# Kernel tuning notes

Measured on AMD Instinct MI355X. Metric: run time of the kernel, lower is better.

## Reference

```python
import jax, jax.numpy as jnp
import numpy as np

N_NODES = 50000


def gcn_conv(x, src, dst, norm, W, b, n_nodes):
    """One GCNConv layer: out = scatter_add(norm * (x @ W)[src] -> dst) + b.
    src/dst already include self loops; norm is the symmetric D^-1/2 A_hat D^-1/2 edge weight."""
    h = x @ W  # [N, C_out]
    msg = h[src] * norm[:, None]  # [E+N, C_out]
    out = jax.ops.segment_sum(msg, dst, num_segments=n_nodes)
    return out + b


def build_norm(edge_index, n_nodes):
    """Add self loops and compute symmetric GCN normalization (PyG GCNConv default)."""
    loop = jnp.arange(n_nodes, dtype=edge_index.dtype)
    src = jnp.concatenate([edge_index[0], loop])
    dst = jnp.concatenate([edge_index[1], loop])
    deg = jax.ops.segment_sum(jnp.ones_like(dst, dtype=jnp.float32), dst, num_segments=n_nodes)
    dinv = jnp.where(deg > 0, jax.lax.rsqrt(jnp.maximum(deg, 1.0)), 0.0)
    norm = dinv[src] * dinv[dst]
    return src, dst, norm


def setup_inputs() -> dict:
    key = jax.random.key(0)
    ks = jax.random.split(key, 8)
    in_c, h1, h2, out_c = 768, 256, 128, 2
    x = jax.random.normal(ks[0], (N_NODES, in_c), dtype=jnp.float32)
    edge_index = jax.random.randint(ks[1], (2, 800000), 0, N_NODES, dtype=jnp.int32)
    W1 = jax.random.normal(ks[2], (in_c, h1), dtype=jnp.float32) * 0.02
    b1 = jnp.zeros((h1,), dtype=jnp.float32)
    W2 = jax.random.normal(ks[3], (h1, h2), dtype=jnp.float32) * 0.02
    b2 = jnp.zeros((h2,), dtype=jnp.float32)
    W3 = jax.random.normal(ks[4], (h2, out_c), dtype=jnp.float32) * 0.02
    b3 = jnp.zeros((out_c,), dtype=jnp.float32)
    return {"x": x, "edge_index": edge_index, "W1": W1, "b1": b1,
            "W2": W2, "b2": b2, "W3": W3, "b3": b3}


def reference(x, edge_index, W1, b1, W2, b2, W3, b3):
    n = x.shape[0]
    src, dst, norm = build_norm(edge_index, n)
    # Dropout is identity in eval mode (training=False), so it is omitted.
    h = jax.nn.relu(gcn_conv(x, src, dst, norm, W1, b1, n))
    h = jax.nn.relu(gcn_conv(h, src, dst, norm, W2, b2, n))
    h = gcn_conv(h, src, dst, norm, W3, b3, n)
    return jax.nn.sigmoid(h)
```

## Files before the change

### kernel.cpp

```cpp
#include <hip/hip_runtime.h>
#include <math.h>

typedef short s16x8 __attribute__((ext_vector_type(8)));
typedef __bf16 b16x8 __attribute__((ext_vector_type(8)));
typedef float f32x4 __attribute__((ext_vector_type(4)));
typedef float f32x2 __attribute__((ext_vector_type(2)));
typedef unsigned int u32x4 __attribute__((ext_vector_type(4)));

__device__ inline short f2bf(float f) {
    unsigned u = __float_as_uint(f);
    unsigned r = u + 0x7FFFu + ((u >> 16) & 1u);
    return (short)(r >> 16);
}
__device__ inline float bf2f(unsigned short u) {
    return __uint_as_float(((unsigned)u) << 16);
}


__device__ inline void make_wt_elem(const float* __restrict__ W, short* __restrict__ Wt,
                                    int K, int N, int idx) {
    int NB = N >> 7;
    int j = idx & 7;
    int l = (idx >> 3) & 63;
    int nt = (idx >> 9) & 7;
    int rest = idx >> 12;
    int b = rest % NB;
    int c = rest / NB;
    int k = c * 32 + (l >> 4) * 8 + j;
    int n = b * 128 + nt * 16 + (l & 15);
    Wt[idx] = f2bf(W[(size_t)k * N + n]);
}

__global__ void prep_kernel(const int* __restrict__ dst, int* __restrict__ cnt, int E,
                            const float* __restrict__ W1, short* __restrict__ Wt1,
                            const float* __restrict__ W2, short* __restrict__ Wt2,
                            int cb, int w1b) {
    int b = blockIdx.x;
    int tid = threadIdx.x;
    if (b < cb) {
        int e = b * 256 + tid;
        if (e < E) atomicAdd(&cnt[dst[e]], 1);
    } else if (b < cb + w1b) {
        int idx = (b - cb) * 256 + tid;
        make_wt_elem(W1, Wt1, 768, 256, idx);
    } else {
        int idx = (b - cb - w1b) * 256 + tid;
        make_wt_elem(W2, Wt2, 256, 128, idx);
    }
}


__global__ __launch_bounds__(1024) void blockscan_kernel(const int* __restrict__ cnt,
                                                         int* __restrict__ rp,
                                                         int* __restrict__ bsum, int n) {
    __shared__ int sdata[1024];
    int tid = threadIdx.x;
    int i = blockIdx.x * 1024 + tid;
    int v = (i < n) ? cnt[i] : 0;
    sdata[tid] = v;
    __syncthreads();
    for (int off = 1; off < 1024; off <<= 1) {
        int t = 0;
        if (tid >= off) t = sdata[tid - off];
        __syncthreads();
        sdata[tid] += t;
        __syncthreads();
    }
    if (i < n) rp[i] = sdata[tid] - v;
    if (tid == 1023) bsum[blockIdx.x] = sdata[1023];
}

__global__ void topscan_kernel(int* bsum, int nb) {
    int lane = threadIdx.x;
    int carry = 0;
    for (int base = 0; base < nb; base += 64) {
        int idx = base + lane;
        int orig = (idx < nb) ? bsum[idx] : 0;
        int v = orig;
        for (int off = 1; off < 64; off <<= 1) {
            int t = __shfl_up(v, off, 64);
            if (lane >= off) v += t;
        }
        if (idx < nb) bsum[idx] = carry + v - orig;
        carry += __shfl(v, 63, 64);
    }
}

__global__ __launch_bounds__(1024) void fixup_kernel(int* __restrict__ rp,
                                                     const int* __restrict__ bsum,
                                                     const int* __restrict__ cnt,
                                                     int* __restrict__ cursor,
                                                     float* __restrict__ dinv,
                                                     int n, int E) {
    int i = blockIdx.x * 1024 + threadIdx.x;
    if (i < n) {
        int r = rp[i] + bsum[blockIdx.x];
        rp[i] = r;
        cursor[i] = r;
        dinv[i] = rsqrtf((float)cnt[i] + 1.0f);
    }
    if (i == 0) rp[n] = E;
}

__global__ void fill_kernel(const int* __restrict__ src, const int* __restrict__ dst,
                            int* __restrict__ cursor, const float* __restrict__ dinv,
                            int* __restrict__ csrc, float* __restrict__ cw, int E) {
    int e = blockIdx.x * blockDim.x + threadIdx.x;
    if (e >= E) return;
    int d = dst[e];
    int s = src[e];
    int p = atomicAdd(&cursor[d], 1);
    csrc[p] = s;
    cw[p] = dinv[s] * dinv[d];
}


__global__ __launch_bounds__(256, 3) void gemm1_kernel(const float* __restrict__ x,
                                                       const short* __restrict__ Wt,
                                                       unsigned char* __restrict__ h8,
                                                       int M) {
    constexpr int KC = 24;
    constexpr int RT = 2;
    constexpr int O = KC * 4;
    constexpr int F = KC * RT * 64 / 256;

    __shared__ s16x8 As[KC * RT * 64];

    const int tid = threadIdx.x;
    const int m0 = blockIdx.x * (RT * 16);

    s16x8 v[F];
#pragma unroll
    for (int i = 0; i < F; ++i) {
        int idx = i * 256 + tid;
        int r = idx / O;
        int o = idx - r * O;
        int row = m0 + r;
        if (row >= M) row = M - 1;
        const float4* fp = (const float4*)(x + (size_t)row * 768 + o * 8);
        float4 f0 = fp[0];
        float4 f1 = fp[1];
        u32x4 pk;
        pk.x = (__float_as_uint(f0.x) >> 16) | (__float_as_uint(f0.y) & 0xFFFF0000u);
        pk.y = (__float_as_uint(f0.z) >> 16) | (__float_as_uint(f0.w) & 0xFFFF0000u);
        pk.z = (__float_as_uint(f1.x) >> 16) | (__float_as_uint(f1.y) & 0xFFFF0000u);
        pk.w = (__float_as_uint(f1.z) >> 16) | (__float_as_uint(f1.w) & 0xFFFF0000u);
        v[i] = __builtin_bit_cast(s16x8, pk);
    }
#pragma unroll
    for (int i = 0; i < F; ++i) {
        int idx = i * 256 + tid;
        int r = idx / O;
        int o = idx - r * O;
        int c = o >> 2, q = o & 3;
        int slot = q * 16 + (((r & 15) + q + ((c & 3) << 2)) & 15);
        As[(c * RT + (r >> 4)) * 64 + slot] = v[i];
    }
    __syncthreads();

    const int lane = tid & 63;
    const int wave = tid >> 6;
    const int b128 = wave >> 1;
    const int nt0 = (wave & 1) * 4;
    const int q = lane >> 4;
    const int rl = lane & 15;
    const s16x8* wt = (const s16x8*)Wt;

    f32x4 acc[RT][4];
#pragma unroll
    for (int i = 0; i < RT; ++i)
#pragma unroll
        for (int j = 0; j < 4; ++j)
            acc[i][j] = (f32x4){0.f, 0.f, 0.f, 0.f};

#pragma unroll 4
    for (int c = 0; c < KC; ++c) {
        int slot = q * 16 + ((rl + q + ((c & 3) << 2)) & 15);
        b16x8 areg[RT], breg[4];
#pragma unroll
        for (int i = 0; i < RT; ++i)
            areg[i] = __builtin_bit_cast(b16x8, As[(c * RT + i) * 64 + slot]);
        size_t bb = (size_t)(c * 2 + b128) * 512 + nt0 * 64 + lane;
#pragma unroll
        for (int j = 0; j < 4; ++j)
            breg[j] = __builtin_bit_cast(b16x8, wt[bb + j * 64]);
#pragma unroll
        for (int i = 0; i < RT; ++i)
#pragma unroll
            for (int j = 0; j < 4; ++j)
                acc[i][j] = __builtin_amdgcn_mfma_f32_16x16x32_bf16(areg[i], breg[j], acc[i][j], 0, 0, 0);
    }

    const int quad = lane >> 4;
    const int nl = lane & 15;
#pragma unroll
    for (int i = 0; i < RT; ++i) {
        int rbase = m0 + i * 16 + quad * 4;
#pragma unroll
        for (int j = 0; j < 4; ++j) {
            int col = wave * 64 + j * 16 + nl;
#pragma unroll
            for (int r = 0; r < 4; ++r) {
                int row = rbase + r;
                if (row < M) {
                    unsigned u = __builtin_amdgcn_cvt_pk_fp8_f32(acc[i][j][r], acc[i][j][r], 0, false);
                    h8[(size_t)row * 256 + col] = (unsigned char)(u & 0xFF);
                }
            }
        }
    }
}


template<typename AT, int KC, int RT, int CW, int MINW>
__global__ __launch_bounds__(256, MINW) void gemm_panel_kernel(
        const AT* __restrict__ A, const short* __restrict__ Wt,
        unsigned short* __restrict__ Cb, int M) {
    constexpr int K = KC * 32;
    constexpr int O = KC * 4;
    constexpr int F = KC * RT / 4;
    constexpr int NCOLS = CW * 64;
    constexpr int NB = NCOLS >> 7;
    constexpr int MT = RT * CW / 4;

    __shared__ s16x8 As[KC * RT * 64];

    const int tid = threadIdx.x;
    const int m0 = blockIdx.x * (RT * 16);

    s16x8 v[F];
#pragma unroll
    for (int i = 0; i < F; ++i) {
        int idx = i * 256 + tid;
        int r = idx / O;
        int o = idx - r * O;
        int row = m0 + r;
        if (row >= M) row = M - 1;
        v[i] = *(const s16x8*)((const unsigned short*)A + (size_t)row * K + o * 8);
    }
#pragma unroll
    for (int i = 0; i < F; ++i) {
        int idx = i * 256 + tid;
        int r = idx / O;
        int o = idx - r * O;
        int c = o >> 2, q = o & 3;
        int slot = q * 16 + (((r & 15) + q + ((c & 3) << 2)) & 15);
        As[(c * RT + (r >> 4)) * 64 + slot] = v[i];
    }
    __syncthreads();

    const int lane = tid & 63;
    const int wave = tid >> 6;
    const int cw_i = wave % CW;
    const int rg = wave / CW;
    const int mtb = rg * MT;
    const int b128 = (cw_i * 64) >> 7;
    const int nt0 = (cw_i * 4) & 7;
    const int q = lane >> 4;
    const int rl = lane & 15;
    const s16x8* wt = (const s16x8*)Wt;

    f32x4 acc[MT][4];
#pragma unroll
    for (int i = 0; i < MT; ++i)
#pragma unroll
        for (int j = 0; j < 4; ++j)
            acc[i][j] = (f32x4){0.f, 0.f, 0.f, 0.f};

#pragma unroll 4
    for (int c = 0; c < KC; ++c) {
        int slot = q * 16 + ((rl + q + ((c & 3) << 2)) & 15);
        b16x8 areg[MT], breg[4];
#pragma unroll
        for (int i = 0; i < MT; ++i)
            areg[i] = __builtin_bit_cast(b16x8, As[(c * RT + mtb + i) * 64 + slot]);
        size_t bb = (size_t)(c * NB + b128) * 512 + nt0 * 64 + lane;
#pragma unroll
        for (int j = 0; j < 4; ++j)
            breg[j] = __builtin_bit_cast(b16x8, wt[bb + j * 64]);
#pragma unroll
        for (int i = 0; i < MT; ++i)
#pragma unroll
            for (int j = 0; j < 4; ++j)
                acc[i][j] = __builtin_amdgcn_mfma_f32_16x16x32_bf16(areg[i], breg[j], acc[i][j], 0, 0, 0);
    }

    const int quad = lane >> 4;
    const int nl = lane & 15;
#pragma unroll
    for (int i = 0; i < MT; ++i) {
        int rbase = m0 + (mtb + i) * 16 + quad * 4;
#pragma unroll
        for (int j = 0; j < 4; ++j) {
            int col = cw_i * 64 + j * 16 + nl;
#pragma unroll
            for (int rr = 0; rr < 4; ++rr) {
                int row = rbase + rr;
                if (row < M) Cb[(size_t)row * NCOLS + col] = (unsigned short)f2bf(acc[i][j][rr]);
            }
        }
    }
}


__global__ __launch_bounds__(256) void agg256_f8_kernel(const unsigned char* __restrict__ h8,
                                                        const int* __restrict__ rp,
                                                        const int* __restrict__ csrc,
                                                        const float* __restrict__ cw,
                                                        const float* __restrict__ dinv,
                                                        const float* __restrict__ bias,
                                                        unsigned short* __restrict__ out, int n) {
    int node = blockIdx.x * 4 + (threadIdx.x >> 6);
    int lane = threadIdx.x & 63;
    if (node >= n) return;
    const int eg = lane >> 4;
    const int ch = lane & 15;
    float di = dinv[node];

    float acc[16];
    {
        u32x4 v = *(const u32x4*)(h8 + (size_t)node * 256 + ch * 16);
        float ws = (eg == 0) ? di * di : 0.f;
#pragma unroll
        for (int u = 0; u < 4; ++u) {
            f32x2 lo = __builtin_amdgcn_cvt_pk_f32_fp8(v[u], false);
            f32x2 hi = __builtin_amdgcn_cvt_pk_f32_fp8(v[u], true);
            acc[u * 4 + 0] = ws * lo.x; acc[u * 4 + 1] = ws * lo.y;
            acc[u * 4 + 2] = ws * hi.x; acc[u * 4 + 3] = ws * hi.y;
        }
    }

    int e0 = rp[node], e1 = rp[node + 1];
    for (int base = e0; base < e1; base += 64) {
        int idx = base + lane;
        int sb = (idx < e1) ? csrc[idx] : 0;
        float wb = (idx < e1) ? cw[idx] : 0.f;
        int cnt = e1 - base; if (cnt > 64) cnt = 64;
#pragma unroll 2
        for (int i = 0; i < cnt; i += 4) {
            int s = __shfl(sb, i + eg, 64);
            float w = __shfl(wb, i + eg, 64);
            u32x4 v = *(const u32x4*)(h8 + (size_t)s * 256 + ch * 16);
#pragma unroll
            for (int u = 0; u < 4; ++u) {
                f32x2 lo = __builtin_amdgcn_cvt_pk_f32_fp8(v[u], false);
                f32x2 hi = __builtin_amdgcn_cvt_pk_f32_fp8(v[u], true);
                acc[u * 4 + 0] += w * lo.x; acc[u * 4 + 1] += w * lo.y;
                acc[u * 4 + 2] += w * hi.x; acc[u * 4 + 3] += w * hi.y;
            }
        }
    }

#pragma unroll
    for (int k = 0; k < 16; ++k) {
        acc[k] += __shfl_xor(acc[k], 16, 64);
        acc[k] += __shfl_xor(acc[k], 32, 64);
    }

    unsigned pk[8];
#pragma unroll
    for (int k = 0; k < 8; ++k) {
        float4 bv;
        float b0 = bias[ch * 16 + 2 * k];
        float b1 = bias[ch * 16 + 2 * k + 1];
        float a0 = fmaxf(acc[2 * k] + b0, 0.f);
        float a1 = fmaxf(acc[2 * k + 1] + b1, 0.f);
        pk[k] = ((unsigned)(unsigned short)f2bf(a0)) | (((unsigned)(unsigned short)f2bf(a1)) << 16);
        (void)bv;
    }
    if (eg < 2) {
        u32x4 ov;
        ov.x = pk[eg * 4 + 0]; ov.y = pk[eg * 4 + 1];
        ov.z = pk[eg * 4 + 2]; ov.w = pk[eg * 4 + 3];
        *(u32x4*)((char*)out + (size_t)node * 512 + ch * 32 + eg * 16) = ov;
    }
}

__global__ __launch_bounds__(256) void agg128_w3_kernel(const unsigned short* __restrict__ h,
                                                        const int* __restrict__ rp,
                                                        const int* __restrict__ csrc,
                                                        const float* __restrict__ cw,
                                                        const float* __restrict__ dinv,
                                                        const float* __restrict__ b2,
                                                        const float* __restrict__ W3,
                                                        float* __restrict__ z, int n) {
    int node = blockIdx.x * 4 + (threadIdx.x >> 6);
    int lane = threadIdx.x & 63;
    if (node >= n) return;
    const int eg = lane >> 4;
    const int ch = lane & 15;
    float di = dinv[node];

    float acc[8];
    {
        u32x4 v = *(const u32x4*)((const char*)h + (size_t)node * 256 + ch * 16);
        float ws = (eg == 0) ? di * di : 0.f;
#pragma unroll
        for (int u = 0; u < 4; ++u) {
            acc[u * 2 + 0] = ws * __uint_as_float(v[u] << 16);
            acc[u * 2 + 1] = ws * __uint_as_float(v[u] & 0xFFFF0000u);
        }
    }

    int e0 = rp[node], e1 = rp[node + 1];
    for (int base = e0; base < e1; base += 64) {
        int idx = base + lane;
        int sb = (idx < e1) ? csrc[idx] : 0;
        float wb = (idx < e1) ? cw[idx] : 0.f;
        int cnt = e1 - base; if (cnt > 64) cnt = 64;
#pragma unroll 2
        for (int i = 0; i < cnt; i += 4) {
            int s = __shfl(sb, i + eg, 64);
            float w = __shfl(wb, i + eg, 64);
            u32x4 v = *(const u32x4*)((const char*)h + (size_t)s * 256 + ch * 16);
#pragma unroll
            for (int u = 0; u < 4; ++u) {
                acc[u * 2 + 0] += w * __uint_as_float(v[u] << 16);
                acc[u * 2 + 1] += w * __uint_as_float(v[u] & 0xFFFF0000u);
            }
        }
    }

#pragma unroll
    for (int k = 0; k < 8; ++k) {
        acc[k] += __shfl_xor(acc[k], 16, 64);
        acc[k] += __shfl_xor(acc[k], 32, 64);
    }

    float z0 = 0.f, z1 = 0.f;
#pragma unroll
    for (int k = 0; k < 8; ++k) {
        float a = fmaxf(acc[k] + b2[ch * 8 + k], 0.f);
        z0 += a * W3[(ch * 8 + k) * 2];
        z1 += a * W3[(ch * 8 + k) * 2 + 1];
    }
    for (int off = 8; off > 0; off >>= 1) {
        z0 += __shfl_xor(z0, off, 64);
        z1 += __shfl_xor(z1, off, 64);
    }
    if (lane == 0) {
        z[2 * (size_t)node] = z0;
        z[2 * (size_t)node + 1] = z1;
    }
}

__global__ void agg3_kernel(const float* __restrict__ z, const int* __restrict__ rp,
                            const int* __restrict__ csrc, const float* __restrict__ cw,
                            const float* __restrict__ dinv, const float* __restrict__ bias,
                            float* __restrict__ out, int n) {
    int node = blockIdx.x * blockDim.x + threadIdx.x;
    if (node >= n) return;
    float di = dinv[node];
    float a0 = di * di * z[2 * (size_t)node];
    float a1 = di * di * z[2 * (size_t)node + 1];
    int e1 = rp[node + 1];
    for (int e = rp[node]; e < e1; ++e) {
        int s = csrc[e];
        float w = cw[e];
        a0 += w * z[2 * (size_t)s];
        a1 += w * z[2 * (size_t)s + 1];
    }
    a0 += bias[0];
    a1 += bias[1];
    out[2 * (size_t)node]     = 1.f / (1.f + __expf(-a0));
    out[2 * (size_t)node + 1] = 1.f / (1.f + __expf(-a1));
}


extern "C" void kernel_launch(void* const* d_in, const int* in_sizes, int n_in,
                              void* d_out, int out_size, void* d_ws, size_t ws_size,
                              hipStream_t stream) {
    const float* x  = (const float*)d_in[0];
    const int*   ei = (const int*)d_in[1];
    const float* W1 = (const float*)d_in[2];
    const float* b1 = (const float*)d_in[3];
    const float* W2 = (const float*)d_in[4];
    const float* b2 = (const float*)d_in[5];
    const float* W3 = (const float*)d_in[6];
    const float* b3 = (const float*)d_in[7];
    float* out = (float*)d_out;

    const int E  = in_sizes[1] / 2;
    const int C1 = in_sizes[3];
    const int C2 = in_sizes[5];
    const int K1 = in_sizes[2] / C1;
    const int N  = in_sizes[0] / K1;

    const int* srcv = ei;
    const int* dstv = ei + E;

    char* p = (char*)d_ws;
    auto carve = [&](size_t bytes) {
        char* r = p;
        p += (bytes + 255) & ~(size_t)255;
        return r;
    };
    int*   cnt    = (int*)carve((size_t)N * 4);
    int*   rp     = (int*)carve((size_t)(N + 1) * 4);
    int*   cursor = (int*)carve((size_t)N * 4);
    float* dinv   = (float*)carve((size_t)N * 4);
    int*   bsum   = (int*)carve(1024 * 4);
    int*   csrc   = (int*)carve((size_t)E * 4);
    float* cw     = (float*)carve((size_t)E * 4);
    short* Wt1    = (short*)carve((size_t)K1 * C1 * 2);
    short* Wt2    = (short*)carve((size_t)C1 * C2 * 2);
    unsigned char* h8 = (unsigned char*)carve((size_t)N * C1);
    unsigned short* hB = (unsigned short*)carve((size_t)N * C1 * 2);
    unsigned short* h2 = (unsigned short*)carve((size_t)N * C2 * 2);
    float* zbuf   = (float*)carve((size_t)N * 2 * 4);

    const int nb = (N + 1023) / 1024;
    const int cb = (E + 255) / 256;
    const int w1b = (K1 * C1) / 256;
    const int w2b = (C1 * C2) / 256;

    hipMemsetAsync(cnt, 0, (size_t)N * 4, stream);
    prep_kernel<<<cb + w1b + w2b, 256, 0, stream>>>(dstv, cnt, E, W1, Wt1, W2, Wt2, cb, w1b);
    blockscan_kernel<<<nb, 1024, 0, stream>>>(cnt, rp, bsum, N);
    topscan_kernel<<<1, 64, 0, stream>>>(bsum, nb);
    fixup_kernel<<<nb, 1024, 0, stream>>>(rp, bsum, cnt, cursor, dinv, N, E);
    fill_kernel<<<(E + 255) / 256, 256, 0, stream>>>(srcv, dstv, cursor, dinv, csrc, cw, E);

    gemm1_kernel<<<(N + 31) / 32, 256, 0, stream>>>(x, Wt1, h8, N);
    agg256_f8_kernel<<<(N + 3) / 4, 256, 0, stream>>>(h8, rp, csrc, cw, dinv, b1, hB, N);

    gemm_panel_kernel<unsigned short, 8, 4, 2, 4><<<(N + 63) / 64, 256, 0, stream>>>(hB, Wt2, h2, N);
    agg128_w3_kernel<<<(N + 3) / 4, 256, 0, stream>>>(h2, rp, csrc, cw, dinv, b2, W3, zbuf, N);

    agg3_kernel<<<(N + 255) / 256, 256, 0, stream>>>(zbuf, rp, csrc, cw, dinv, b3, out, N);
}
```

Before: 443.0 us.

## Software-pipeline gemm1 with double-buffered LDS A tiles and 64-row blocks

```diff
diff --git a/kernel.cpp b/kernel.cpp
--- a/kernel.cpp
+++ b/kernel.cpp
@@ -115,48 +115,22 @@
 }
 
 
-__global__ __launch_bounds__(256, 3) void gemm1_kernel(const float* __restrict__ x,
+__global__ __launch_bounds__(256, 2) void gemm1_kernel(const float* __restrict__ x,
                                                        const short* __restrict__ Wt,
                                                        unsigned char* __restrict__ h8,
                                                        int M) {
     constexpr int KC = 24;
-    constexpr int RT = 2;
-    constexpr int O = KC * 4;
-    constexpr int F = KC * RT * 64 / 256;
-
-    __shared__ s16x8 As[KC * RT * 64];
+    constexpr int RTB = 4;
+
+    __shared__ s16x8 As[2][RTB * 64];
 
     const int tid = threadIdx.x;
-    const int m0 = blockIdx.x * (RT * 16);
-
-    s16x8 v[F];
-#pragma unroll
-    for (int i = 0; i < F; ++i) {
-        int idx = i * 256 + tid;
-        int r = idx / O;
-        int o = idx - r * O;
-        int row = m0 + r;
-        if (row >= M) row = M - 1;
-        const float4* fp = (const float4*)(x + (size_t)row * 768 + o * 8);
-        float4 f0 = fp[0];
-        float4 f1 = fp[1];
-        u32x4 pk;
-        pk.x = (__float_as_uint(f0.x) >> 16) | (__float_as_uint(f0.y) & 0xFFFF0000u);
-        pk.y = (__float_as_uint(f0.z) >> 16) | (__float_as_uint(f0.w) & 0xFFFF0000u);
-        pk.z = (__float_as_uint(f1.x) >> 16) | (__float_as_uint(f1.y) & 0xFFFF0000u);
-        pk.w = (__float_as_uint(f1.z) >> 16) | (__float_as_uint(f1.w) & 0xFFFF0000u);
-        v[i] = __builtin_bit_cast(s16x8, pk);
-    }
-#pragma unroll
-    for (int i = 0; i < F; ++i) {
-        int idx = i * 256 + tid;
-        int r = idx / O;
-        int o = idx - r * O;
-        int c = o >> 2, q = o & 3;
-        int slot = q * 16 + (((r & 15) + q + ((c & 3) << 2)) & 15);
-        As[(c * RT + (r >> 4)) * 64 + slot] = v[i];
-    }
-    __syncthreads();
+    const int m0 = blockIdx.x * (RTB * 16);
+
+    const int rs = tid >> 2;
+    const int qs = tid & 3;
+    int srow = m0 + rs; if (srow >= M) srow = M - 1;
+    const float4* xrow = (const float4*)(x + (size_t)srow * 768);
 
     const int lane = tid & 63;
     const int wave = tid >> 6;
@@ -166,35 +140,72 @@
     const int rl = lane & 15;
     const s16x8* wt = (const s16x8*)Wt;
 
-    f32x4 acc[RT][4];
-#pragma unroll
-    for (int i = 0; i < RT; ++i)
+    auto loadA = [&](int c) -> s16x8 {
+        float4 f0 = xrow[c * 8 + qs * 2];
+        float4 f1 = xrow[c * 8 + qs * 2 + 1];
+        u32x4 pk;
+        pk.x = (__float_as_uint(f0.x) >> 16) | (__float_as_uint(f0.y) & 0xFFFF0000u);
+        pk.y = (__float_as_uint(f0.z) >> 16) | (__float_as_uint(f0.w) & 0xFFFF0000u);
+        pk.z = (__float_as_uint(f1.x) >> 16) | (__float_as_uint(f1.y) & 0xFFFF0000u);
+        pk.w = (__float_as_uint(f1.z) >> 16) | (__float_as_uint(f1.w) & 0xFFFF0000u);
+        return __builtin_bit_cast(s16x8, pk);
+    };
+    auto writeA = [&](int c, int buf, s16x8 v) {
+        int slot = qs * 16 + (((rs & 15) + qs + ((c & 3) << 2)) & 15);
+        As[buf][(rs >> 4) * 64 + slot] = v;
+    };
+    auto loadB = [&](int c, b16x8* breg) {
+        size_t bb = (size_t)(c * 2 + b128) * 512 + nt0 * 64 + lane;
+#pragma unroll
+        for (int j = 0; j < 4; ++j)
+            breg[j] = __builtin_bit_cast(b16x8, wt[bb + j * 64]);
+    };
+
+    f32x4 acc[RTB][4];
+#pragma unroll
+    for (int i = 0; i < RTB; ++i)
 #pragma unroll
         for (int j = 0; j < 4; ++j)
             acc[i][j] = (f32x4){0.f, 0.f, 0.f, 0.f};
 
-#pragma unroll 4
+    b16x8 bcur[4], bnext[4];
+    {
+        s16x8 va = loadA(0);
+        loadB(0, bcur);
+        writeA(0, 0, va);
+    }
+    __syncthreads();
+
+#pragma unroll 2
     for (int c = 0; c < KC; ++c) {
+        s16x8 vn;
+        if (c + 1 < KC) {
+            vn = loadA(c + 1);
+            loadB(c + 1, bnext);
+        }
         int slot = q * 16 + ((rl + q + ((c & 3) << 2)) & 15);
-        b16x8 areg[RT], breg[4];
-#pragma unroll
-        for (int i = 0; i < RT; ++i)
-            areg[i] = __builtin_bit_cast(b16x8, As[(c * RT + i) * 64 + slot]);
-        size_t bb = (size_t)(c * 2 + b128) * 512 + nt0 * 64 + lane;
-#pragma unroll
-        for (int j = 0; j < 4; ++j)
-            breg[j] = __builtin_bit_cast(b16x8, wt[bb + j * 64]);
-#pragma unroll
-        for (int i = 0; i < RT; ++i)
+        b16x8 areg[RTB];
+#pragma unroll
+        for (int i = 0; i < RTB; ++i)
+            areg[i] = __builtin_bit_cast(b16x8, As[c & 1][i * 64 + slot]);
+#pragma unroll
+        for (int i = 0; i < RTB; ++i)
 #pragma unroll
             for (int j = 0; j < 4; ++j)
-                acc[i][j] = __builtin_amdgcn_mfma_f32_16x16x32_bf16(areg[i], breg[j], acc[i][j], 0, 0, 0);
+                acc[i][j] = __builtin_amdgcn_mfma_f32_16x16x32_bf16(areg[i], bcur[j], acc[i][j], 0, 0, 0);
+        if (c + 1 < KC) {
+            __syncthreads();
+            writeA(c + 1, (c + 1) & 1, vn);
+#pragma unroll
+            for (int j = 0; j < 4; ++j) bcur[j] = bnext[j];
+            __syncthreads();
+        }
     }
 
     const int quad = lane >> 4;
     const int nl = lane & 15;
 #pragma unroll
-    for (int i = 0; i < RT; ++i) {
+    for (int i = 0; i < RTB; ++i) {
         int rbase = m0 + i * 16 + quad * 4;
 #pragma unroll
         for (int j = 0; j < 4; ++j) {
@@ -360,13 +371,11 @@
     unsigned pk[8];
 #pragma unroll
     for (int k = 0; k < 8; ++k) {
-        float4 bv;
         float b0 = bias[ch * 16 + 2 * k];
         float b1 = bias[ch * 16 + 2 * k + 1];
         float a0 = fmaxf(acc[2 * k] + b0, 0.f);
         float a1 = fmaxf(acc[2 * k + 1] + b1, 0.f);
         pk[k] = ((unsigned)(unsigned short)f2bf(a0)) | (((unsigned)(unsigned short)f2bf(a1)) << 16);
-        (void)bv;
     }
     if (eg < 2) {
         u32x4 ov;
@@ -521,7 +530,7 @@
     fixup_kernel<<<nb, 1024, 0, stream>>>(rp, bsum, cnt, cursor, dinv, N, E);
     fill_kernel<<<(E + 255) / 256, 256, 0, stream>>>(srcv, dstv, cursor, dinv, csrc, cw, E);
 
-    gemm1_kernel<<<(N + 31) / 32, 256, 0, stream>>>(x, Wt1, h8, N);
+    gemm1_kernel<<<(N + 63) / 64, 256, 0, stream>>>(x, Wt1, h8, N);
     agg256_f8_kernel<<<(N + 3) / 4, 256, 0, stream>>>(h8, rp, csrc, cw, dinv, b1, hB, N);
 
     gemm_panel_kernel<unsigned short, 8, 4, 2, 4><<<(N + 63) / 64, 256, 0, stream>>>(hB, Wt2, h2, N);
```

Result: no change. 450.8 us (+1.8%).

## Switch first-layer GEMM to FP8 MFMA with 64-row tiles

Applied to the files above, without the earlier changes.

```diff
diff --git a/kernel.cpp b/kernel.cpp
--- a/kernel.cpp
+++ b/kernel.cpp
@@ -6,6 +6,8 @@
 typedef float f32x4 __attribute__((ext_vector_type(4)));
 typedef float f32x2 __attribute__((ext_vector_type(2)));
 typedef unsigned int u32x4 __attribute__((ext_vector_type(4)));
+typedef unsigned int u32x2 __attribute__((ext_vector_type(2)));
+typedef unsigned long u64x2 __attribute__((ext_vector_type(2)));
 
 __device__ inline short f2bf(float f) {
     unsigned u = __float_as_uint(f);
@@ -32,7 +34,7 @@
 }
 
 __global__ void prep_kernel(const int* __restrict__ dst, int* __restrict__ cnt, int E,
-                            const float* __restrict__ W1, short* __restrict__ Wt1,
+                            const float* __restrict__ W1, unsigned char* __restrict__ Wt1,
                             const float* __restrict__ W2, short* __restrict__ Wt2,
                             int cb, int w1b) {
     int b = blockIdx.x;
@@ -42,7 +44,16 @@
         if (e < E) atomicAdd(&cnt[dst[e]], 1);
     } else if (b < cb + w1b) {
         int idx = (b - cb) * 256 + tid;
-        make_wt_elem(W1, Wt1, 768, 256, idx);
+        int j = idx & 7;
+        int t = (idx >> 3) & 3;
+        int l = (idx >> 5) & 63;
+        int cw = (idx >> 11) & 3;
+        int c = idx >> 13;
+        int k = c * 32 + (l >> 4) * 8 + j;
+        int n = cw * 64 + t * 16 + (l & 15);
+        float v = W1[(size_t)k * 256 + n];
+        unsigned u = __builtin_amdgcn_cvt_pk_fp8_f32(v, v, 0u, false);
+        Wt1[idx] = (unsigned char)(u & 0xFF);
     } else {
         int idx = (b - cb - w1b) * 256 + tid;
         make_wt_elem(W2, Wt2, 256, 128, idx);
@@ -116,55 +127,41 @@
 
 
 __global__ __launch_bounds__(256, 3) void gemm1_kernel(const float* __restrict__ x,
-                                                       const short* __restrict__ Wt,
+                                                       const unsigned char* __restrict__ Wt,
                                                        unsigned char* __restrict__ h8,
                                                        int M) {
     constexpr int KC = 24;
-    constexpr int RT = 2;
-    constexpr int O = KC * 4;
-    constexpr int F = KC * RT * 64 / 256;
-
-    __shared__ s16x8 As[KC * RT * 64];
+    constexpr int RT = 4;
+
+    __shared__ u32x2 As[KC * RT * 64];
 
     const int tid = threadIdx.x;
-    const int m0 = blockIdx.x * (RT * 16);
-
-    s16x8 v[F];
-#pragma unroll
-    for (int i = 0; i < F; ++i) {
+    const int m0 = blockIdx.x * 64;
+
+#pragma unroll 4
+    for (int i = 0; i < 24; ++i) {
         int idx = i * 256 + tid;
-        int r = idx / O;
-        int o = idx - r * O;
+        int r = idx / 96;
+        int o = idx - r * 96;
         int row = m0 + r;
         if (row >= M) row = M - 1;
         const float4* fp = (const float4*)(x + (size_t)row * 768 + o * 8);
         float4 f0 = fp[0];
         float4 f1 = fp[1];
-        u32x4 pk;
-        pk.x = (__float_as_uint(f0.x) >> 16) | (__float_as_uint(f0.y) & 0xFFFF0000u);
-        pk.y = (__float_as_uint(f0.z) >> 16) | (__float_as_uint(f0.w) & 0xFFFF0000u);
-        pk.z = (__float_as_uint(f1.x) >> 16) | (__float_as_uint(f1.y) & 0xFFFF0000u);
-        pk.w = (__float_as_uint(f1.z) >> 16) | (__float_as_uint(f1.w) & 0xFFFF0000u);
-        v[i] = __builtin_bit_cast(s16x8, pk);
-    }
-#pragma unroll
-    for (int i = 0; i < F; ++i) {
-        int idx = i * 256 + tid;
-        int r = idx / O;
-        int o = idx - r * O;
+        unsigned w0 = __builtin_amdgcn_cvt_pk_fp8_f32(f0.x, f0.y, 0u, false);
+        w0 = __builtin_amdgcn_cvt_pk_fp8_f32(f0.z, f0.w, w0, true);
+        unsigned w1 = __builtin_amdgcn_cvt_pk_fp8_f32(f1.x, f1.y, 0u, false);
+        w1 = __builtin_amdgcn_cvt_pk_fp8_f32(f1.z, f1.w, w1, true);
         int c = o >> 2, q = o & 3;
         int slot = q * 16 + (((r & 15) + q + ((c & 3) << 2)) & 15);
-        As[(c * RT + (r >> 4)) * 64 + slot] = v[i];
+        As[(c * RT + (r >> 4)) * 64 + slot] = (u32x2){w0, w1};
     }
     __syncthreads();
 
     const int lane = tid & 63;
-    const int wave = tid >> 6;
-    const int b128 = wave >> 1;
-    const int nt0 = (wave & 1) * 4;
+    const int cw = tid >> 6;
     const int q = lane >> 4;
     const int rl = lane & 15;
-    const s16x8* wt = (const s16x8*)Wt;
 
     f32x4 acc[RT][4];
 #pragma unroll
@@ -176,19 +173,21 @@
 #pragma unroll 4
     for (int c = 0; c < KC; ++c) {
         int slot = q * 16 + ((rl + q + ((c & 3) << 2)) & 15);
-        b16x8 areg[RT], breg[4];
+        long a8[RT];
 #pragma unroll
         for (int i = 0; i < RT; ++i)
-            areg[i] = __builtin_bit_cast(b16x8, As[(c * RT + i) * 64 + slot]);
-        size_t bb = (size_t)(c * 2 + b128) * 512 + nt0 * 64 + lane;
-#pragma unroll
-        for (int j = 0; j < 4; ++j)
-            breg[j] = __builtin_bit_cast(b16x8, wt[bb + j * 64]);
+            a8[i] = __builtin_bit_cast(long, As[(c * RT + i) * 64 + slot]);
+        const char* bp = (const char*)Wt + ((size_t)(c * 4 + cw) * 64 + lane) * 32;
+        u64x2 B0 = *(const u64x2*)bp;
+        u64x2 B1 = *(const u64x2*)(bp + 16);
+        long b8[4];
+        b8[0] = (long)B0.x; b8[1] = (long)B0.y;
+        b8[2] = (long)B1.x; b8[3] = (long)B1.y;
 #pragma unroll
         for (int i = 0; i < RT; ++i)
 #pragma unroll
             for (int j = 0; j < 4; ++j)
-                acc[i][j] = __builtin_amdgcn_mfma_f32_16x16x32_bf16(areg[i], breg[j], acc[i][j], 0, 0, 0);
+                acc[i][j] = __builtin_amdgcn_mfma_f32_16x16x32_fp8_fp8(a8[i], b8[j], acc[i][j], 0, 0, 0);
     }
 
     const int quad = lane >> 4;
@@ -198,7 +197,7 @@
         int rbase = m0 + i * 16 + quad * 4;
 #pragma unroll
         for (int j = 0; j < 4; ++j) {
-            int col = wave * 64 + j * 16 + nl;
+            int col = cw * 64 + j * 16 + nl;
 #pragma unroll
             for (int r = 0; r < 4; ++r) {
                 int row = rbase + r;
@@ -360,13 +359,11 @@
     unsigned pk[8];
 #pragma unroll
     for (int k = 0; k < 8; ++k) {
-        float4 bv;
         float b0 = bias[ch * 16 + 2 * k];
         float b1 = bias[ch * 16 + 2 * k + 1];
         float a0 = fmaxf(acc[2 * k] + b0, 0.f);
         float a1 = fmaxf(acc[2 * k + 1] + b1, 0.f);
         pk[k] = ((unsigned)(unsigned short)f2bf(a0)) | (((unsigned)(unsigned short)f2bf(a1)) << 16);
-        (void)bv;
     }
     if (eg < 2) {
         u32x4 ov;
@@ -502,7 +499,7 @@
     int*   bsum   = (int*)carve(1024 * 4);
     int*   csrc   = (int*)carve((size_t)E * 4);
     float* cw     = (float*)carve((size_t)E * 4);
-    short* Wt1    = (short*)carve((size_t)K1 * C1 * 2);
+    unsigned char* Wt1 = (unsigned char*)carve((size_t)K1 * C1);
     short* Wt2    = (short*)carve((size_t)C1 * C2 * 2);
     unsigned char* h8 = (unsigned char*)carve((size_t)N * C1);
     unsigned short* hB = (unsigned short*)carve((size_t)N * C1 * 2);
@@ -521,7 +518,7 @@
     fixup_kernel<<<nb, 1024, 0, stream>>>(rp, bsum, cnt, cursor, dinv, N, E);
     fill_kernel<<<(E + 255) / 256, 256, 0, stream>>>(srcv, dstv, cursor, dinv, csrc, cw, E);
 
-    gemm1_kernel<<<(N + 31) / 32, 256, 0, stream>>>(x, Wt1, h8, N);
+    gemm1_kernel<<<(N + 63) / 64, 256, 0, stream>>>(x, Wt1, h8, N);
     agg256_f8_kernel<<<(N + 3) / 4, 256, 0, stream>>>(h8, rp, csrc, cw, dinv, b1, hB, N);
 
     gemm_panel_kernel<unsigned short, 8, 4, 2, 4><<<(N + 63) / 64, 256, 0, stream>>>(hB, Wt2, h2, N);
```

Result: no change. 451.1 us (+1.8%).
